# Kernel optimization log

Hardware: AMD Instinct MI355X
Metric: run time of the kernel (lower is better)

## Reference

```python
import jax, jax.numpy as jnp
import numpy as np


def setup_inputs() -> dict:
    key = jax.random.key(0)
    ks = jax.random.split(key, 6)
    B, L, N, C, D = 8, 512, 2048, 1024, 128
    return {
        "teacher_logits": jax.random.normal(ks[0], (B, L, N), dtype=jnp.float32),
        "teacher_features": jax.random.normal(ks[1], (B, N, C), dtype=jnp.float32),
        "Wq": jax.random.normal(ks[2], (D, C), dtype=jnp.float32) * (1.0 / np.sqrt(C)),
        "bq": jnp.zeros((D,), dtype=jnp.float32),
        "Wk": jax.random.normal(ks[3], (D, C), dtype=jnp.float32) * (1.0 / np.sqrt(C)),
        "bk": jnp.zeros((D,), dtype=jnp.float32),
    }


def reference(teacher_logits, teacher_features, Wq, bq, Wk, bk):
    # Linear projections (torch nn.Linear: x @ W^T + b)
    query = jnp.einsum("bnc,dc->bnd", teacher_features, Wq) + bq  # [B,N,D]
    key = jnp.einsum("bnc,dc->bnd", teacher_features, Wk) + bk    # [B,N,D]
    energy = jnp.einsum("bnd,bmd->bnm", query, key)               # [B,N,N]
    attention = jax.nn.softmax(energy, axis=-1)                   # softmax over last dim
    # x_m = teacher_logits @ attention^T : [B,L,N] x [B,N,N]^T -> [B,L,N]
    x_m = jnp.einsum("bln,bmn->blm", teacher_logits, attention)
    return x_m
```

## Files before the change

### kernel.cpp

```cpp
#include <hip/hip_runtime.h>
#include <hip/hip_bf16.h>

#define B_ 8
#define L_ 512
#define N_ 2048
#define C_ 1024
#define D_ 128

typedef __attribute__((ext_vector_type(8))) short    short8;
typedef __attribute__((ext_vector_type(4))) short    short4v;
typedef __attribute__((ext_vector_type(8))) _Float16 half8;
typedef __attribute__((ext_vector_type(4))) float    floatx4;

static __device__ __forceinline__ float s2f(short s) {
    return __uint_as_float(((unsigned)(unsigned short)s) << 16);
}
static __device__ __forceinline__ short f2bf(float f) {
    union { __hip_bfloat16 h; short s; } u;
    u.h = __float2bfloat16(f);
    return u.s;
}

struct F8 { float v[8]; };

static __device__ __forceinline__ F8 load8(const void* raw, long off, int is_bf16) {
    F8 r;
    if (is_bf16) {
        short8 x = *reinterpret_cast<const short8*>((const short*)raw + off);
        #pragma unroll
        for (int i = 0; i < 8; ++i) r.v[i] = s2f(x[i]);
    } else {
        const float* p = (const float*)raw + off;
        float4 a = *reinterpret_cast<const float4*>(p);
        float4 b = *reinterpret_cast<const float4*>(p + 4);
        r.v[0]=a.x; r.v[1]=a.y; r.v[2]=a.z; r.v[3]=a.w;
        r.v[4]=b.x; r.v[5]=b.y; r.v[6]=b.z; r.v[7]=b.w;
    }
    return r;
}

static __device__ __forceinline__ float bias_at(const void* raw, int d, int is_bf16) {
    return is_bf16 ? s2f(((const short*)raw)[d]) : ((const float*)raw)[d];
}

static __device__ __forceinline__ void load_lds16(const void* g, void* l) {
    __builtin_amdgcn_global_load_lds(
        (const __attribute__((address_space(1))) void*)g,
        (__attribute__((address_space(3))) void*)l, 16, 0, 0);
}

__global__ void detect_kernel(const unsigned* __restrict__ words, int* __restrict__ flag) {
    int cnt = 0;
    for (int i = threadIdx.x; i < 256; i += 64) {
        float lowv = __uint_as_float(words[i] << 16);
        float a = fabsf(lowv);
        if (a >= 1e-5f && a <= 100.0f) cnt++;
    }
    #pragma unroll
    for (int off = 32; off; off >>= 1) cnt += __shfl_down(cnt, off);
    if (threadIdx.x == 0) flag[0] = (cnt > 128) ? 1 : 0;
}

__global__ __launch_bounds__(256) void cvt_kernel(const void* __restrict__ in_raw,
                                                  short* __restrict__ out, long n,
                                                  const int* __restrict__ flag) {
    if (*flag) return;
    long i = ((long)blockIdx.x * 256 + threadIdx.x) * 8;
    if (i >= n) return;
    F8 x = load8(in_raw, i, 0);
    short8 o;
    #pragma unroll
    for (int j = 0; j < 8; ++j) o[j] = f2bf(x.v[j]);
    *reinterpret_cast<short8*>(out + i) = o;
}

__global__ __launch_bounds__(256) void cvt_half2_kernel(
    const void* __restrict__ a_raw, _Float16* __restrict__ a_out,
    const void* __restrict__ b_raw, _Float16* __restrict__ b_out,
    long n, const int* __restrict__ flag) {
    if (*flag) return;
    const void* in  = blockIdx.y ? b_raw : a_raw;
    _Float16*   out = blockIdx.y ? b_out : a_out;
    long i = ((long)blockIdx.x * 256 + threadIdx.x) * 8;
    if (i >= n) return;
    F8 x = load8(in, i, 0);
    half8 o;
    #pragma unroll
    for (int j = 0; j < 8; ++j) o[j] = (_Float16)x.v[j];
    *reinterpret_cast<half8*>(out + i) = o;
}

__global__ __launch_bounds__(512) void proj_kernel(
    const void* __restrict__ Fraw,
    const void* __restrict__ Wq_raw, const void* __restrict__ Wk_raw,
    const _Float16* __restrict__ Wq_h, const _Float16* __restrict__ Wk_h,
    const void* __restrict__ bq_raw, const void* __restrict__ bk_raw,
    _Float16* __restrict__ Q, _Float16* __restrict__ K,
    const int* __restrict__ flag)
{
    const int is_bf16 = *flag;
    const int tid  = threadIdx.x;
    const int wave = tid >> 6;
    const int lane = tid & 63;
    const int quad = lane >> 4;
    const int l16  = lane & 15;
    const long r0  = (long)blockIdx.x * 64;

    const int m0   = (wave & 1) * 32;
    const int col0 = (wave >> 1) * 64;

    __shared__ short Ft[2][64 * 64];
    __shared__ short Wt[2][256 * 64];

    floatx4 acc[2][4] = {};

    const int srow  = lane >> 3;
    const int sslot = lane & 7;
    const int skoff = (sslot ^ srow) * 8;

    if (is_bf16) {
        const short* Fr  = (const short*)Fraw;
        const short* Wqr = (const short*)Wq_raw;
        const short* Wkr = (const short*)Wk_raw;

        auto STAGE = [&](int kb, int buf) {
            const int k0 = kb * 64;
            #pragma unroll
            for (int j = 0; j < 4; ++j) {
                const int c = wave * 4 + j;
                const short* Wr = (c < 16) ? Wqr : Wkr;
                const int wrow = (c & 15) * 8 + srow;
                load_lds16(Wr + (long)wrow * C_ + k0 + skoff,
                           Wt[buf] + c * 512 + lane * 8);
            }
            load_lds16(Fr + (r0 + wave * 8 + srow) * (long)C_ + k0 + skoff,
                       Ft[buf] + wave * 512 + lane * 8);
        };

        STAGE(0, 0);
        __syncthreads();
        for (int kb = 0; kb < 16; ++kb) {
            const int buf = kb & 1;
            if (kb < 15) STAGE(kb + 1, buf ^ 1);
            #pragma unroll
            for (int kk = 0; kk < 2; ++kk) {
                short8 af[2], bfr[4];
                #pragma unroll
                for (int t = 0; t < 2; ++t) {
                    const int row = m0 + t * 16 + l16;
                    const int ph  = (kk * 4 + quad) ^ (row & 7);
                    af[t] = *reinterpret_cast<const short8*>(Ft[buf] + row * 64 + ph * 8);
                }
                #pragma unroll
                for (int u = 0; u < 4; ++u) {
                    const int wrow = col0 + u * 16 + l16;
                    const int ph   = (kk * 4 + quad) ^ (wrow & 7);
                    bfr[u] = *reinterpret_cast<const short8*>(Wt[buf] + wrow * 64 + ph * 8);
                }
                #pragma unroll
                for (int t = 0; t < 2; ++t)
                    #pragma unroll
                    for (int u = 0; u < 4; ++u)
                        acc[t][u] = __builtin_amdgcn_mfma_f32_16x16x32_bf16(af[t], bfr[u], acc[t][u], 0, 0, 0);
            }
            __syncthreads();
        }
    } else {
        _Float16* FtH0 = (_Float16*)Ft[0];
        _Float16* FtH1 = (_Float16*)Ft[1];
        _Float16* WtH0 = (_Float16*)Wt[0];
        _Float16* WtH1 = (_Float16*)Wt[1];

        const int frow = tid >> 3;
        const int fseg = tid & 7;
        const int fph  = fseg ^ (frow & 7);

        auto STAGE = [&](int kb, int buf) {
            const int k0 = kb * 64;
            _Float16* Wth = buf ? WtH1 : WtH0;
            _Float16* Fth = buf ? FtH1 : FtH0;
            #pragma unroll
            for (int j = 0; j < 4; ++j) {
                const int c = wave * 4 + j;
                const _Float16* Wh = (c < 16) ? Wq_h : Wk_h;
                const int wrow = (c & 15) * 8 + srow;
                load_lds16(Wh + (long)wrow * C_ + k0 + skoff,
                           Wth + c * 512 + lane * 8);
            }
            F8 x = load8(Fraw, (r0 + frow) * (long)C_ + k0 + fseg * 8, 0);
            half8 h;
            #pragma unroll
            for (int j = 0; j < 8; ++j) h[j] = (_Float16)x.v[j];
            *reinterpret_cast<half8*>(Fth + frow * 64 + fph * 8) = h;
        };

        STAGE(0, 0);
        __syncthreads();
        for (int kb = 0; kb < 16; ++kb) {
            const int buf = kb & 1;
            if (kb < 15) STAGE(kb + 1, buf ^ 1);
            _Float16* Wth = buf ? WtH1 : WtH0;
            _Float16* Fth = buf ? FtH1 : FtH0;
            #pragma unroll
            for (int kk = 0; kk < 2; ++kk) {
                half8 af[2], bfr[4];
                #pragma unroll
                for (int t = 0; t < 2; ++t) {
                    const int row = m0 + t * 16 + l16;
                    const int ph  = (kk * 4 + quad) ^ (row & 7);
                    af[t] = *reinterpret_cast<const half8*>(Fth + row * 64 + ph * 8);
                }
                #pragma unroll
                for (int u = 0; u < 4; ++u) {
                    const int wrow = col0 + u * 16 + l16;
                    const int ph   = (kk * 4 + quad) ^ (wrow & 7);
                    bfr[u] = *reinterpret_cast<const half8*>(Wth + wrow * 64 + ph * 8);
                }
                #pragma unroll
                for (int t = 0; t < 2; ++t)
                    #pragma unroll
                    for (int u = 0; u < 4; ++u)
                        acc[t][u] = __builtin_amdgcn_mfma_f32_16x16x32_f16(af[t], bfr[u], acc[t][u], 0, 0, 0);
            }
            __syncthreads();
        }
    }

    const bool isK = (col0 >= 128);
    const void* braw = isK ? bk_raw : bq_raw;
    _Float16* Out    = isK ? K : Q;
    #pragma unroll
    for (int u = 0; u < 4; ++u) {
        const int d = (col0 + u * 16 + l16) & 127;
        const float bv = bias_at(braw, d, is_bf16);
        #pragma unroll
        for (int t = 0; t < 2; ++t)
            #pragma unroll
            for (int r = 0; r < 4; ++r) {
                const long row = r0 + m0 + t * 16 + quad * 4 + r;
                Out[row * D_ + d] = (_Float16)(acc[t][u][r] + bv);
            }
    }
}

__global__ __launch_bounds__(512, 2) void fused_attn_xm_kernel(
    const void* __restrict__ Lraw,
    const short* __restrict__ Lcvt,
    const _Float16* __restrict__ Q,
    const _Float16* __restrict__ K,
    void* __restrict__ OutRaw,
    const int* __restrict__ flag)
{
    const int is_bf16 = *flag;
    const int f    = blockIdx.y * 32 + blockIdx.x;
    const int b    = f & 7;
    const int m0   = (f >> 3) * 64;
    const int wave = threadIdx.x >> 6;
    const int lane = threadIdx.x & 63;
    const int quad = lane >> 4;
    const int l16  = lane & 15;

    __shared__ short P0[64 * 128];
    __shared__ short P1[64 * 128];
    __shared__ float Zs[64];

    if (threadIdx.x < 64) Zs[threadIdx.x] = 0.0f;

    const short*    Lb = (is_bf16 ? (const short*)Lraw : Lcvt) + (long)b * L_ * N_;
    const _Float16* Qb = Q + (long)b * N_ * D_;
    const _Float16* Kb = K + (long)b * N_ * D_;

    half8 bq[4][4];
    #pragma unroll
    for (int u = 0; u < 4; ++u)
        #pragma unroll
        for (int s = 0; s < 4; ++s)
            bq[u][s] = *reinterpret_cast<const half8*>(
                Qb + (long)(m0 + u * 16 + l16) * D_ + s * 32 + quad * 8);

    const int lw  = wave * 64;
    const int swz = l16 * 2;
    const short* Lw = Lb + (long)(lw + l16) * N_ + quad * 8;
    const _Float16* Kw = Kb + (long)(wave * 16 + l16) * D_ + quad * 8;
    const int pwr = ((wave * 4 + quad) ^ swz) << 2;

    floatx4 acc[4][4] = {};
    float zpart[4] = {};

    for (int ch = 0; ch < 16; ++ch) {
        const int n0 = ch * 128;
        short* Pb = (ch & 1) ? P1 : P0;

        const _Float16* krow = Kw + (long)n0 * D_;
        half8 kf[4];
        #pragma unroll
        for (int s = 0; s < 4; ++s)
            kf[s] = *reinterpret_cast<const half8*>(krow + s * 32);

        short8 al[4][4];
        #pragma unroll
        for (int t = 0; t < 4; ++t)
            #pragma unroll
            for (int ks = 0; ks < 4; ++ks)
                al[t][ks] = *reinterpret_cast<const short8*>(
                    Lw + (long)t * 16 * N_ + n0 + ks * 32);

        floatx4 ae[4] = {};
        #pragma unroll
        for (int s = 0; s < 4; ++s)
            #pragma unroll
            for (int u = 0; u < 4; ++u)
                ae[u] = __builtin_amdgcn_mfma_f32_16x16x32_f16(kf[s], bq[u][s], ae[u], 0, 0, 0);

        #pragma unroll
        for (int u = 0; u < 4; ++u) {
            short4v pk;
            #pragma unroll
            for (int r = 0; r < 4; ++r) {
                float e = __expf(ae[u][r]);
                zpart[u] += e;
                pk[r] = f2bf(e);
            }
            *reinterpret_cast<short4v*>(Pb + (u * 16 + l16) * 128 + pwr) = pk;
        }
        __syncthreads();

        #pragma unroll
        for (int ks = 0; ks < 4; ++ks) {
            short8 bp[4];
            #pragma unroll
            for (int u = 0; u < 4; ++u) {
                const int m = u * 16 + l16;
                bp[u] = *reinterpret_cast<const short8*>(
                    Pb + m * 128 + ((((ks * 8 + quad * 2) ^ swz)) << 2));
            }
            #pragma unroll
            for (int t = 0; t < 4; ++t)
                #pragma unroll
                for (int u = 0; u < 4; ++u)
                    acc[t][u] = __builtin_amdgcn_mfma_f32_16x16x32_bf16(
                        al[t][ks], bp[u], acc[t][u], 0, 0, 0);
        }
    }

    #pragma unroll
    for (int u = 0; u < 4; ++u) {
        float z = zpart[u];
        z += __shfl_xor(z, 16);
        z += __shfl_xor(z, 32);
        if (lane < 16) atomicAdd(&Zs[u * 16 + lane], z);
    }
    __syncthreads();

    float invz[4];
    #pragma unroll
    for (int u = 0; u < 4; ++u) invz[u] = 1.0f / Zs[u * 16 + l16];

    if (is_bf16) {
        short* Ob = (short*)OutRaw + (long)b * L_ * N_;
        #pragma unroll
        for (int t = 0; t < 4; ++t)
            #pragma unroll
            for (int u = 0; u < 4; ++u)
                #pragma unroll
                for (int r = 0; r < 4; ++r) {
                    const long row = lw + t * 16 + quad * 4 + r;
                    const int  col = m0 + u * 16 + l16;
                    Ob[row * N_ + col] = f2bf(acc[t][u][r] * invz[u]);
                }
    } else {
        float* Ob = (float*)OutRaw + (long)b * L_ * N_;
        #pragma unroll
        for (int t = 0; t < 4; ++t)
            #pragma unroll
            for (int u = 0; u < 4; ++u)
                #pragma unroll
                for (int r = 0; r < 4; ++r) {
                    const long row = lw + t * 16 + quad * 4 + r;
                    const int  col = m0 + u * 16 + l16;
                    Ob[row * N_ + col] = acc[t][u][r] * invz[u];
                }
    }
}

extern "C" void kernel_launch(void* const* d_in, const int* in_sizes, int n_in,
                              void* d_out, int out_size, void* d_ws, size_t ws_size,
                              hipStream_t stream) {
    const void* logits_raw = d_in[0];
    const void* feats_raw  = d_in[1];
    const void* wq_raw     = d_in[2];
    const void* bq_raw     = d_in[3];
    const void* wk_raw     = d_in[4];
    const void* bk_raw     = d_in[5];

    char* ws = (char*)d_ws;
    size_t off = 0;
    int* flag = (int*)(ws + off);           off += 256;
    short* logb = (short*)(ws + off);       off += (size_t)B_ * L_ * N_ * 2;
    _Float16* Wq_h = (_Float16*)(ws + off); off += (size_t)D_ * C_ * 2;
    _Float16* Wk_h = (_Float16*)(ws + off); off += (size_t)D_ * C_ * 2;
    _Float16* Q = (_Float16*)(ws + off);    off += (size_t)B_ * N_ * D_ * 2;
    _Float16* K = (_Float16*)(ws + off);    off += (size_t)B_ * N_ * D_ * 2;

    hipLaunchKernelGGL(detect_kernel, dim3(1), dim3(64), 0, stream,
                       (const unsigned*)feats_raw, flag);
    hipLaunchKernelGGL(cvt_kernel, dim3((B_ * L_ * N_) / (256 * 8)), dim3(256), 0, stream,
                       logits_raw, logb, (long)B_ * L_ * N_, flag);
    hipLaunchKernelGGL(cvt_half2_kernel, dim3((D_ * C_) / (256 * 8), 2), dim3(256), 0, stream,
                       wq_raw, Wq_h, wk_raw, Wk_h, (long)D_ * C_, flag);
    hipLaunchKernelGGL(proj_kernel, dim3(B_ * N_ / 64), dim3(512), 0, stream,
                       feats_raw, wq_raw, wk_raw, Wq_h, Wk_h, bq_raw, bk_raw, Q, K, flag);
    hipLaunchKernelGGL(fused_attn_xm_kernel, dim3(N_ / 64, B_), dim3(512), 0, stream,
                       logits_raw, logb, Q, K, d_out, flag);
}
```

Before: 229.7 us.

## Fold dtype detection into kernels, merge conversions, split projection grid by Q/K

Drops the separate detect kernel and has every block recompute the dtype flag from the feature words in shared memory. The logits and weight conversion kernels become a single launch. The projection kernel now uses a 2D grid with one block per Q or K, halving per-block LDS and accumulators and raising its occupancy hint to 4, so more blocks can be resident. This removes two launches and the global flag dependency, at the cost of redundant detection work per block and features being read twice in projection.

```diff
diff --git a/kernel.cpp b/kernel.cpp
--- a/kernel.cpp
+++ b/kernel.cpp
@@ -49,56 +49,68 @@
         (__attribute__((address_space(3))) void*)l, 16, 0, 0);
 }
 
-__global__ void detect_kernel(const unsigned* __restrict__ words, int* __restrict__ flag) {
-    int cnt = 0;
-    for (int i = threadIdx.x; i < 256; i += 64) {
-        float lowv = __uint_as_float(words[i] << 16);
-        float a = fabsf(lowv);
-        if (a >= 1e-5f && a <= 100.0f) cnt++;
-    }
-    #pragma unroll
-    for (int off = 32; off; off >>= 1) cnt += __shfl_down(cnt, off);
-    if (threadIdx.x == 0) flag[0] = (cnt > 128) ? 1 : 0;
-}
-
-__global__ __launch_bounds__(256) void cvt_kernel(const void* __restrict__ in_raw,
-                                                  short* __restrict__ out, long n,
-                                                  const int* __restrict__ flag) {
-    if (*flag) return;
-    long i = ((long)blockIdx.x * 256 + threadIdx.x) * 8;
-    if (i >= n) return;
-    F8 x = load8(in_raw, i, 0);
-    short8 o;
-    #pragma unroll
-    for (int j = 0; j < 8; ++j) o[j] = f2bf(x.v[j]);
-    *reinterpret_cast<short8*>(out + i) = o;
-}
-
-__global__ __launch_bounds__(256) void cvt_half2_kernel(
-    const void* __restrict__ a_raw, _Float16* __restrict__ a_out,
-    const void* __restrict__ b_raw, _Float16* __restrict__ b_out,
-    long n, const int* __restrict__ flag) {
-    if (*flag) return;
-    const void* in  = blockIdx.y ? b_raw : a_raw;
-    _Float16*   out = blockIdx.y ? b_out : a_out;
-    long i = ((long)blockIdx.x * 256 + threadIdx.x) * 8;
-    if (i >= n) return;
-    F8 x = load8(in, i, 0);
-    half8 o;
-    #pragma unroll
-    for (int j = 0; j < 8; ++j) o[j] = (_Float16)x.v[j];
-    *reinterpret_cast<half8*>(out + i) = o;
-}
-
-__global__ __launch_bounds__(512) void proj_kernel(
+static __device__ __forceinline__ int detect_flag(const unsigned* __restrict__ w) {
+    __shared__ int sflag;
+    const int tid = threadIdx.x;
+    if (tid < 64) {
+        int cnt = 0;
+        for (int i = tid; i < 256; i += 64) {
+            float lowv = __uint_as_float(w[i] << 16);
+            float a = fabsf(lowv);
+            if (a >= 1e-5f && a <= 100.0f) cnt++;
+        }
+        #pragma unroll
+        for (int off = 32; off; off >>= 1) cnt += __shfl_down(cnt, off);
+        if (tid == 0) sflag = (cnt > 128) ? 1 : 0;
+    }
+    __syncthreads();
+    return sflag;
+}
+
+__global__ __launch_bounds__(256) void cvtall_kernel(
+    const unsigned* __restrict__ dw,
+    const void* __restrict__ logits_raw, short* __restrict__ logb,
+    const void* __restrict__ wq_raw, _Float16* __restrict__ Wq_h,
+    const void* __restrict__ wk_raw, _Float16* __restrict__ Wk_h)
+{
+    const int fl = detect_flag(dw);
+    if (fl) return;
+    const long LBLK = (long)B_ * L_ * N_ / (256 * 8);
+    const long WBLK = (long)D_ * C_ / (256 * 8);
+    const long blk = blockIdx.x;
+    if (blk < LBLK) {
+        long i = blk * 2048 + (long)threadIdx.x * 8;
+        F8 x = load8(logits_raw, i, 0);
+        short8 o;
+        #pragma unroll
+        for (int j = 0; j < 8; ++j) o[j] = f2bf(x.v[j]);
+        *reinterpret_cast<short8*>(logb + i) = o;
+    } else if (blk < LBLK + WBLK) {
+        long i = (blk - LBLK) * 2048 + (long)threadIdx.x * 8;
+        F8 x = load8(wq_raw, i, 0);
+        half8 o;
+        #pragma unroll
+        for (int j = 0; j < 8; ++j) o[j] = (_Float16)x.v[j];
+        *reinterpret_cast<half8*>(Wq_h + i) = o;
+    } else {
+        long i = (blk - LBLK - WBLK) * 2048 + (long)threadIdx.x * 8;
+        F8 x = load8(wk_raw, i, 0);
+        half8 o;
+        #pragma unroll
+        for (int j = 0; j < 8; ++j) o[j] = (_Float16)x.v[j];
+        *reinterpret_cast<half8*>(Wk_h + i) = o;
+    }
+}
+
+__global__ __launch_bounds__(512, 4) void proj_kernel(
     const void* __restrict__ Fraw,
     const void* __restrict__ Wq_raw, const void* __restrict__ Wk_raw,
     const _Float16* __restrict__ Wq_h, const _Float16* __restrict__ Wk_h,
     const void* __restrict__ bq_raw, const void* __restrict__ bk_raw,
-    _Float16* __restrict__ Q, _Float16* __restrict__ K,
-    const int* __restrict__ flag)
+    _Float16* __restrict__ Q, _Float16* __restrict__ K)
 {
-    const int is_bf16 = *flag;
+    const int is_bf16 = detect_flag((const unsigned*)Fraw);
+    const int isK  = blockIdx.y;
     const int tid  = threadIdx.x;
     const int wave = tid >> 6;
     const int lane = tid & 63;
@@ -107,29 +119,27 @@
     const long r0  = (long)blockIdx.x * 64;
 
     const int m0   = (wave & 1) * 32;
-    const int col0 = (wave >> 1) * 64;
+    const int col0 = (wave >> 1) * 32;
 
     __shared__ short Ft[2][64 * 64];
-    __shared__ short Wt[2][256 * 64];
-
-    floatx4 acc[2][4] = {};
+    __shared__ short Wt[2][128 * 64];
+
+    floatx4 acc[2][2] = {};
 
     const int srow  = lane >> 3;
     const int sslot = lane & 7;
     const int skoff = (sslot ^ srow) * 8;
 
     if (is_bf16) {
-        const short* Fr  = (const short*)Fraw;
-        const short* Wqr = (const short*)Wq_raw;
-        const short* Wkr = (const short*)Wk_raw;
+        const short* Fr = (const short*)Fraw;
+        const short* Wr = (const short*)(isK ? Wk_raw : Wq_raw);
 
         auto STAGE = [&](int kb, int buf) {
             const int k0 = kb * 64;
             #pragma unroll
-            for (int j = 0; j < 4; ++j) {
-                const int c = wave * 4 + j;
-                const short* Wr = (c < 16) ? Wqr : Wkr;
-                const int wrow = (c & 15) * 8 + srow;
+            for (int j = 0; j < 2; ++j) {
+                const int c = wave * 2 + j;
+                const int wrow = c * 8 + srow;
                 load_lds16(Wr + (long)wrow * C_ + k0 + skoff,
                            Wt[buf] + c * 512 + lane * 8);
             }
@@ -144,7 +154,7 @@
             if (kb < 15) STAGE(kb + 1, buf ^ 1);
             #pragma unroll
             for (int kk = 0; kk < 2; ++kk) {
-                short8 af[2], bfr[4];
+                short8 af[2], bfr[2];
                 #pragma unroll
                 for (int t = 0; t < 2; ++t) {
                     const int row = m0 + t * 16 + l16;
@@ -152,7 +162,7 @@
                     af[t] = *reinterpret_cast<const short8*>(Ft[buf] + row * 64 + ph * 8);
                 }
                 #pragma unroll
-                for (int u = 0; u < 4; ++u) {
+                for (int u = 0; u < 2; ++u) {
                     const int wrow = col0 + u * 16 + l16;
                     const int ph   = (kk * 4 + quad) ^ (wrow & 7);
                     bfr[u] = *reinterpret_cast<const short8*>(Wt[buf] + wrow * 64 + ph * 8);
@@ -160,12 +170,28 @@
                 #pragma unroll
                 for (int t = 0; t < 2; ++t)
                     #pragma unroll
-                    for (int u = 0; u < 4; ++u)
+                    for (int u = 0; u < 2; ++u)
                         acc[t][u] = __builtin_amdgcn_mfma_f32_16x16x32_bf16(af[t], bfr[u], acc[t][u], 0, 0, 0);
             }
             __syncthreads();
         }
+
+        const void* braw = isK ? bk_raw : bq_raw;
+        _Float16* Out    = isK ? K : Q;
+        #pragma unroll
+        for (int u = 0; u < 2; ++u) {
+            const int d = col0 + u * 16 + l16;
+            const float bv = bias_at(braw, d, 1);
+            #pragma unroll
+            for (int t = 0; t < 2; ++t)
+                #pragma unroll
+                for (int r = 0; r < 4; ++r) {
+                    const long row = r0 + m0 + t * 16 + quad * 4 + r;
+                    Out[row * D_ + d] = (_Float16)(acc[t][u][r] + bv);
+                }
+        }
     } else {
+        const _Float16* Wh = isK ? Wk_h : Wq_h;
         _Float16* FtH0 = (_Float16*)Ft[0];
         _Float16* FtH1 = (_Float16*)Ft[1];
         _Float16* WtH0 = (_Float16*)Wt[0];
@@ -180,10 +206,9 @@
             _Float16* Wth = buf ? WtH1 : WtH0;
             _Float16* Fth = buf ? FtH1 : FtH0;
             #pragma unroll
-            for (int j = 0; j < 4; ++j) {
-                const int c = wave * 4 + j;
-                const _Float16* Wh = (c < 16) ? Wq_h : Wk_h;
-                const int wrow = (c & 15) * 8 + srow;
+            for (int j = 0; j < 2; ++j) {
+                const int c = wave * 2 + j;
+                const int wrow = c * 8 + srow;
                 load_lds16(Wh + (long)wrow * C_ + k0 + skoff,
                            Wth + c * 512 + lane * 8);
             }
@@ -203,7 +228,7 @@
             _Float16* Fth = buf ? FtH1 : FtH0;
             #pragma unroll
             for (int kk = 0; kk < 2; ++kk) {
-                half8 af[2], bfr[4];
+                half8 af[2], bfr[2];
                 #pragma unroll
                 for (int t = 0; t < 2; ++t) {
                     const int row = m0 + t * 16 + l16;
@@ -211,7 +236,7 @@
                     af[t] = *reinterpret_cast<const half8*>(Fth + row * 64 + ph * 8);
                 }
                 #pragma unroll
-                for (int u = 0; u < 4; ++u) {
+                for (int u = 0; u < 2; ++u) {
                     const int wrow = col0 + u * 16 + l16;
                     const int ph   = (kk * 4 + quad) ^ (wrow & 7);
                     bfr[u] = *reinterpret_cast<const half8*>(Wth + wrow * 64 + ph * 8);
@@ -219,27 +244,26 @@
                 #pragma unroll
                 for (int t = 0; t < 2; ++t)
                     #pragma unroll
-                    for (int u = 0; u < 4; ++u)
+                    for (int u = 0; u < 2; ++u)
                         acc[t][u] = __builtin_amdgcn_mfma_f32_16x16x32_f16(af[t], bfr[u], acc[t][u], 0, 0, 0);
             }
             __syncthreads();
         }
-    }
-
-    const bool isK = (col0 >= 128);
-    const void* braw = isK ? bk_raw : bq_raw;
-    _Float16* Out    = isK ? K : Q;
-    #pragma unroll
-    for (int u = 0; u < 4; ++u) {
-        const int d = (col0 + u * 16 + l16) & 127;
-        const float bv = bias_at(braw, d, is_bf16);
-        #pragma unroll
-        for (int t = 0; t < 2; ++t)
-            #pragma unroll
-            for (int r = 0; r < 4; ++r) {
-                const long row = r0 + m0 + t * 16 + quad * 4 + r;
-                Out[row * D_ + d] = (_Float16)(acc[t][u][r] + bv);
-            }
+
+        const void* braw = isK ? bk_raw : bq_raw;
+        _Float16* Out    = isK ? K : Q;
+        #pragma unroll
+        for (int u = 0; u < 2; ++u) {
+            const int d = col0 + u * 16 + l16;
+            const float bv = bias_at(braw, d, 0);
+            #pragma unroll
+            for (int t = 0; t < 2; ++t)
+                #pragma unroll
+                for (int r = 0; r < 4; ++r) {
+                    const long row = r0 + m0 + t * 16 + quad * 4 + r;
+                    Out[row * D_ + d] = (_Float16)(acc[t][u][r] + bv);
+                }
+        }
     }
 }
 
@@ -249,9 +273,8 @@
     const _Float16* __restrict__ Q,
     const _Float16* __restrict__ K,
     void* __restrict__ OutRaw,
-    const int* __restrict__ flag)
+    const unsigned* __restrict__ dw)
 {
-    const int is_bf16 = *flag;
     const int f    = blockIdx.y * 32 + blockIdx.x;
     const int b    = f & 7;
     const int m0   = (f >> 3) * 64;
@@ -265,6 +288,7 @@
     __shared__ float Zs[64];
 
     if (threadIdx.x < 64) Zs[threadIdx.x] = 0.0f;
+    const int is_bf16 = detect_flag(dw);
 
     const short*    Lb = (is_bf16 ? (const short*)Lraw : Lcvt) + (long)b * L_ * N_;
     const _Float16* Qb = Q + (long)b * N_ * D_;
@@ -395,21 +419,18 @@
 
     char* ws = (char*)d_ws;
     size_t off = 0;
-    int* flag = (int*)(ws + off);           off += 256;
+    off += 256;
     short* logb = (short*)(ws + off);       off += (size_t)B_ * L_ * N_ * 2;
     _Float16* Wq_h = (_Float16*)(ws + off); off += (size_t)D_ * C_ * 2;
     _Float16* Wk_h = (_Float16*)(ws + off); off += (size_t)D_ * C_ * 2;
     _Float16* Q = (_Float16*)(ws + off);    off += (size_t)B_ * N_ * D_ * 2;
     _Float16* K = (_Float16*)(ws + off);    off += (size_t)B_ * N_ * D_ * 2;
 
-    hipLaunchKernelGGL(detect_kernel, dim3(1), dim3(64), 0, stream,
-                       (const unsigned*)feats_raw, flag);
-    hipLaunchKernelGGL(cvt_kernel, dim3((B_ * L_ * N_) / (256 * 8)), dim3(256), 0, stream,
-                       logits_raw, logb, (long)B_ * L_ * N_, flag);
-    hipLaunchKernelGGL(cvt_half2_kernel, dim3((D_ * C_) / (256 * 8), 2), dim3(256), 0, stream,
-                       wq_raw, Wq_h, wk_raw, Wk_h, (long)D_ * C_, flag);
-    hipLaunchKernelGGL(proj_kernel, dim3(B_ * N_ / 64), dim3(512), 0, stream,
-                       feats_raw, wq_raw, wk_raw, Wq_h, Wk_h, bq_raw, bk_raw, Q, K, flag);
+    hipLaunchKernelGGL(cvtall_kernel, dim3(4096 + 64 + 64), dim3(256), 0, stream,
+                       (const unsigned*)feats_raw, logits_raw, logb,
+                       wq_raw, Wq_h, wk_raw, Wk_h);
+    hipLaunchKernelGGL(proj_kernel, dim3(B_ * N_ / 64, 2), dim3(512), 0, stream,
+                       feats_raw, wq_raw, wk_raw, Wq_h, Wk_h, bq_raw, bk_raw, Q, K);
     hipLaunchKernelGGL(fused_attn_xm_kernel, dim3(N_ / 64, B_), dim3(512), 0, stream,
-                       logits_raw, logb, Q, K, d_out, flag);
-}
+                       logits_raw, logb, Q, K, d_out, (const unsigned*)feats_raw);
+}
```

Measured after the change: 228.5 us. Within noise of the previous version (-0.6%).
